# Kernel optimization log

Measured on AMD Instinct MI355X. Metric: run time of the kernel, lower is better.

Reference implementation:

```python
import jax, jax.numpy as jnp
import numpy as np

SEQ_LEN = 512
MAX_SPAN = 15
BATCH = 8
HIDDEN = 1024
WIDTH_DIM = 64
NUM_LABELS = 3


def _enumerate_spans(seq_len, max_span):
    starts, ends = [], []
    for s in range(seq_len):
        for e in range(s, min(s + max_span, seq_len)):
            starts.append(s)
            ends.append(e)
    return np.asarray(starts, np.int32), np.asarray(ends, np.int32)


def setup_inputs() -> dict:
    key = jax.random.key(0)
    k = jax.random.split(key, 6)
    starts, ends = _enumerate_spans(SEQ_LEN, MAX_SPAN)  # N = 7575
    d_in = HIDDEN * 2 + WIDTH_DIM  # 2112
    return {
        "sequence_output": jax.random.normal(k[0], (BATCH, SEQ_LEN, HIDDEN), jnp.float32),
        "width_emb": jax.random.normal(k[1], (MAX_SPAN, WIDTH_DIM), jnp.float32) * 0.02,
        "W1": jax.random.normal(k[2], (d_in, HIDDEN), jnp.float32) * (1.0 / np.sqrt(d_in)),
        "b1": jnp.zeros((HIDDEN,), jnp.float32),
        "W2": jax.random.normal(k[3], (HIDDEN, NUM_LABELS), jnp.float32) * (1.0 / np.sqrt(HIDDEN)),
        "b2": jnp.zeros((NUM_LABELS,), jnp.float32),
        "span_starts": jnp.asarray(starts),
        "span_ends": jnp.asarray(ends),
    }


def reference(sequence_output, width_emb, W1, b1, W2, b2, span_starts, span_ends):
    # Gather start/end token representations for every candidate span.
    B = sequence_output.shape[0]
    N = span_starts.shape[0]
    start_repr = sequence_output[:, span_starts]            # [B, N, H]
    end_repr = sequence_output[:, span_ends]                # [B, N, H]
    width_repr = width_emb[span_ends - span_starts]         # [N, 64]
    width_repr = jnp.broadcast_to(width_repr[None], (B, N, width_repr.shape[-1]))
    span_reprs = jnp.concatenate([start_repr, end_repr, width_repr], axis=-1)  # [B, N, 2H+64]
    # Span classifier MLP (dropout is identity in eval mode).
    h = jax.nn.relu(jnp.einsum("bnd,dh->bnh", span_reprs, W1) + b1)
    logits = jnp.einsum("bnh,hl->bnl", h, W2) + b2          # [B, N, num_labels]
    return logits
```

## Files before the change

### kernel.cpp

```cpp
#include <hip/hip_runtime.h>
#include <stdint.h>

#define SEQ 512
#define BATCH 8
#define HID 1024

typedef __attribute__((ext_vector_type(8))) __bf16 bf16x8;
typedef __attribute__((ext_vector_type(4))) float f32x4;

__device__ __forceinline__ unsigned short f2bf(float f) {
    unsigned int u = __float_as_uint(f);
    unsigned int r = 0x7fffu + ((u >> 16) & 1u);
    return (unsigned short)((u + r) >> 16);
}

__device__ __forceinline__ void unpack8(uint4 v, float* f) {
    f[0] = __uint_as_float(v.x << 16);
    f[1] = __uint_as_float(v.x & 0xffff0000u);
    f[2] = __uint_as_float(v.y << 16);
    f[3] = __uint_as_float(v.y & 0xffff0000u);
    f[4] = __uint_as_float(v.z << 16);
    f[5] = __uint_as_float(v.z & 0xffff0000u);
    f[6] = __uint_as_float(v.w << 16);
    f[7] = __uint_as_float(v.w & 0xffff0000u);
}

__global__ __launch_bounds__(256) void k_prep(const float* __restrict__ seq,
                                              const float* __restrict__ wemb,
                                              const float* __restrict__ W1,
                                              const float* __restrict__ b1,
                                              ushort* __restrict__ seqb,
                                              ushort* __restrict__ Bt,
                                              ushort* __restrict__ Rbf) {
    __shared__ float tile[32][33];
    const int bid = blockIdx.x;
    const int tid = threadIdx.x;
    if (bid < 4096) {
        int i = bid * 256 + tid;
        float4 v = ((const float4*)seq)[i];
        ushort4 o;
        o.x = f2bf(v.x); o.y = f2bf(v.y); o.z = f2bf(v.z); o.w = f2bf(v.w);
        ((ushort4*)seqb)[i] = o;
    } else if (bid < 6144) {
        int idx = bid - 4096;
        int nb = (idx & 63) * 32, kb = (idx >> 6) * 32;
        int tx = tid & 31, ty = tid >> 5;
        int n = nb + tx;
        int rb = (n < 1024) ? 0 : 1024;
        int nc = n - rb;
#pragma unroll
        for (int i = 0; i < 4; ++i) {
            int k = kb + ty + i * 8;
            tile[ty + i * 8][tx] = W1[(size_t)(rb + k) * 1024 + nc];
        }
        __syncthreads();
#pragma unroll
        for (int i = 0; i < 4; ++i) {
            int n2 = nb + ty + i * 8;
            Bt[(size_t)n2 * 1024 + kb + tx] = f2bf(tile[tx][ty + i * 8]);
        }
    } else {
        int idx = (bid - 6144) * 256 + tid;
        int w = idx >> 10, j = idx & 1023;
        float acc = b1[j];
#pragma unroll
        for (int c = 0; c < 64; ++c)
            acc = fmaf(wemb[w * 64 + c], W1[(size_t)(2048 + c) * 1024 + j], acc);
        Rbf[idx] = f2bf(acc);
    }
}

__global__ __launch_bounds__(256) void k_gemm(const ushort* __restrict__ A,
                                              const ushort* __restrict__ Bt,
                                              ushort* __restrict__ P,
                                              ushort* __restrict__ Q) {
    __shared__ ushort Al[2 * 128 * 32];
    __shared__ ushort Bl[2 * 128 * 32];
    const int tid = threadIdx.x;
    const int wid = tid >> 6;
    const int lane = tid & 63;
    const int bid = blockIdx.x;
    const int swz = ((bid & 7) << 6) | (bid >> 3);
    const int n0 = (swz & 15) * 128;
    const int m0 = (swz >> 4) * 128;
    const int wm = (wid >> 1) * 64;
    const int wn = (wid & 1) * 64;
    const int srow = lane >> 2;
    const int scol = (lane & 3) * 8;
    const int fr = lane & 15;
    const int fk = (lane >> 4) * 8;

    f32x4 acc[4][4] = {};

    for (int k0 = 0; k0 < 1024; k0 += 64) {
#pragma unroll
        for (int r = 0; r < 4; ++r) {
            int c = wid + 4 * r;
            int half = c >> 3;
            int rows = (c & 7) * 16;
            const ushort* sa = A  + (size_t)(m0 + rows + srow) * 1024 + k0 + half * 32 + scol;
            const ushort* sb = Bt + (size_t)(n0 + rows + srow) * 1024 + k0 + half * 32 + scol;
            int loff = half * 4096 + rows * 32;
            __builtin_amdgcn_global_load_lds((const __attribute__((address_space(1))) void*)sa,
                                             (__attribute__((address_space(3))) void*)(Al + loff),
                                             16, 0, 0);
            __builtin_amdgcn_global_load_lds((const __attribute__((address_space(1))) void*)sb,
                                             (__attribute__((address_space(3))) void*)(Bl + loff),
                                             16, 0, 0);
        }
        __syncthreads();
#pragma unroll
        for (int kk = 0; kk < 2; ++kk) {
            bf16x8 af[4], bg[4];
#pragma unroll
            for (int i = 0; i < 4; ++i) {
                af[i] = *(const bf16x8*)(Al + kk * 4096 + (wm + i * 16 + fr) * 32 + fk);
                bg[i] = *(const bf16x8*)(Bl + kk * 4096 + (wn + i * 16 + fr) * 32 + fk);
            }
#pragma unroll
            for (int i = 0; i < 4; ++i)
#pragma unroll
                for (int j = 0; j < 4; ++j)
                    acc[i][j] = __builtin_amdgcn_mfma_f32_16x16x32_bf16(af[i], bg[j], acc[i][j], 0, 0, 0);
        }
        __syncthreads();
    }

    ushort* Cb = (n0 < 1024) ? P : Q;
    const int nc0 = n0 & 1023;
    const int cr = (lane >> 4) * 4;
    const int cc = lane & 15;
#pragma unroll
    for (int i = 0; i < 4; ++i)
#pragma unroll
        for (int j = 0; j < 4; ++j) {
            ushort* Cp = Cb + (size_t)(m0 + wm + i * 16 + cr) * 1024 + (nc0 + wn + j * 16 + cc);
#pragma unroll
            for (int r = 0; r < 4; ++r)
                Cp[(size_t)r * 1024] = f2bf(acc[i][j][r]);
        }
}

__global__ __launch_bounds__(1024) void k_span2(const ushort* __restrict__ Pmat,
                                                const ushort* __restrict__ Qmat,
                                                const ushort* __restrict__ Rbf,
                                                const float* __restrict__ W2,
                                                const float* __restrict__ b2,
                                                float* __restrict__ out, int nspans) {
    __shared__ ushort Qs[30 * 1024];
    __shared__ ushort Rs[15 * 1024];
    const int tid = threadIdx.x;
    const int wid = tid >> 6, lane = tid & 63;
    const int b = blockIdx.x >> 5;
    const int s0 = (blockIdx.x & 31) << 4;

#pragma unroll
    for (int i = 0; i < 4; ++i) {
        int c = wid + (i << 4);
        if (c < 60) {
            int g = (c << 9) + lane * 8;
            int row = s0 + (g >> 10);
            if (row > SEQ - 1) row = SEQ - 1;
            const ushort* src = Qmat + (((size_t)(b << 9) + row) << 10) + (g & 1023);
            __builtin_amdgcn_global_load_lds((const __attribute__((address_space(1))) void*)src,
                                             (__attribute__((address_space(3))) void*)(Qs + (c << 9)),
                                             16, 0, 0);
        }
    }
#pragma unroll
    for (int i = 0; i < 2; ++i) {
        int c = wid + (i << 4);
        if (c < 30) {
            int g = (c << 9) + lane * 8;
            __builtin_amdgcn_global_load_lds((const __attribute__((address_space(1))) void*)(Rbf + g),
                                             (__attribute__((address_space(3))) void*)(Rs + (c << 9)),
                                             16, 0, 0);
        }
    }

    float w2r[3][2][8];
#pragma unroll
    for (int it = 0; it < 2; ++it)
#pragma unroll
        for (int u = 0; u < 8; ++u) {
            int j = lane * 8 + it * 512 + u;
            w2r[0][it][u] = W2[j * 3 + 0];
            w2r[1][it][u] = W2[j * 3 + 1];
            w2r[2][it][u] = W2[j * 3 + 2];
        }
    const float bb0 = b2[0], bb1 = b2[1], bb2 = b2[2];

    const int s = s0 + wid;
    float pf[16];
    {
        const uint4* pr = (const uint4*)(Pmat + (((size_t)(b << 9) + s) << 10) + lane * 8);
        unpack8(pr[0], pf);
        unpack8(pr[64], pf + 8);
    }

    __syncthreads();

    const int rrem = SEQ - s;
    const int nsp = (rrem < 15) ? rrem : 15;
    const int off = (rrem >= 15) ? 15 * s : (7575 - (rrem * (rrem + 1)) / 2);
    float* op = out + ((size_t)b * nspans + off) * 3;

    for (int w = 0; w < nsp; ++w) {
        const int erow = wid + w;
        float a0 = 0.f, a1 = 0.f, a2 = 0.f;
#pragma unroll
        for (int it = 0; it < 2; ++it) {
            uint4 qv = *(const uint4*)((const char*)Qs + erow * 2048 + it * 1024 + lane * 16);
            uint4 rv = *(const uint4*)((const char*)Rs + w * 2048 + it * 1024 + lane * 16);
            float qf[8], rf[8];
            unpack8(qv, qf);
            unpack8(rv, rf);
#pragma unroll
            for (int u = 0; u < 8; ++u) {
                float h = pf[it * 8 + u] + qf[u] + rf[u];
                h = fmaxf(h, 0.f);
                a0 = fmaf(h, w2r[0][it][u], a0);
                a1 = fmaf(h, w2r[1][it][u], a1);
                a2 = fmaf(h, w2r[2][it][u], a2);
            }
        }
#pragma unroll
        for (int o = 32; o; o >>= 1) {
            a0 += __shfl_xor(a0, o);
            a1 += __shfl_xor(a1, o);
            a2 += __shfl_xor(a2, o);
        }
        if (lane == 0) {
            op[w * 3 + 0] = a0 + bb0;
            op[w * 3 + 1] = a1 + bb1;
            op[w * 3 + 2] = a2 + bb2;
        }
    }
}

extern "C" void kernel_launch(void* const* d_in, const int* in_sizes, int n_in,
                              void* d_out, int out_size, void* d_ws, size_t ws_size,
                              hipStream_t stream) {
    const float* seq    = (const float*)d_in[0];
    const float* wemb   = (const float*)d_in[1];
    const float* W1     = (const float*)d_in[2];
    const float* b1     = (const float*)d_in[3];
    const float* W2     = (const float*)d_in[4];
    const float* b2     = (const float*)d_in[5];
    float* out = (float*)d_out;
    int nspans = in_sizes[6];

    char* ws = (char*)d_ws;
    ushort* seqb = (ushort*)ws;
    ushort* Bt   = (ushort*)(ws + (8u << 20));
    ushort* Pmat = (ushort*)(ws + (12u << 20));
    ushort* Qmat = (ushort*)(ws + (20u << 20));
    ushort* Rbf  = (ushort*)(ws + (28u << 20));

    hipLaunchKernelGGL(k_prep, dim3(6204), dim3(256), 0, stream,
                       seq, wemb, W1, b1, seqb, Bt, Rbf);
    hipLaunchKernelGGL(k_gemm, dim3(512), dim3(256), 0, stream, seqb, Bt, Pmat, Qmat);
    hipLaunchKernelGGL(k_span2, dim3(BATCH * (SEQ / 16)), dim3(1024), 0, stream,
                       Pmat, Qmat, Rbf, W2, b2, out, nspans);
}
```

Before: 62.69 us.

## Double-buffer GEMM LDS tiles and use 8 warps per block

```diff
diff --git a/kernel.cpp b/kernel.cpp
--- a/kernel.cpp
+++ b/kernel.cpp
@@ -70,12 +70,12 @@
     }
 }
 
-__global__ __launch_bounds__(256) void k_gemm(const ushort* __restrict__ A,
+__global__ __launch_bounds__(512) void k_gemm(const ushort* __restrict__ A,
                                               const ushort* __restrict__ Bt,
                                               ushort* __restrict__ P,
                                               ushort* __restrict__ Q) {
-    __shared__ ushort Al[2 * 128 * 32];
-    __shared__ ushort Bl[2 * 128 * 32];
+    __shared__ ushort Al[2][8192];
+    __shared__ ushort Bl[2][8192];
     const int tid = threadIdx.x;
     const int wid = tid >> 6;
     const int lane = tid & 63;
@@ -83,48 +83,61 @@
     const int swz = ((bid & 7) << 6) | (bid >> 3);
     const int n0 = (swz & 15) * 128;
     const int m0 = (swz >> 4) * 128;
-    const int wm = (wid >> 1) * 64;
-    const int wn = (wid & 1) * 64;
+    const int wm = (wid >> 2) * 64;
+    const int wn = (wid & 3) * 32;
     const int srow = lane >> 2;
     const int scol = (lane & 3) * 8;
     const int fr = lane & 15;
     const int fk = (lane >> 4) * 8;
 
-    f32x4 acc[4][4] = {};
-
-    for (int k0 = 0; k0 < 1024; k0 += 64) {
-#pragma unroll
-        for (int r = 0; r < 4; ++r) {
-            int c = wid + 4 * r;
-            int half = c >> 3;
-            int rows = (c & 7) * 16;
-            const ushort* sa = A  + (size_t)(m0 + rows + srow) * 1024 + k0 + half * 32 + scol;
-            const ushort* sb = Bt + (size_t)(n0 + rows + srow) * 1024 + k0 + half * 32 + scol;
-            int loff = half * 4096 + rows * 32;
-            __builtin_amdgcn_global_load_lds((const __attribute__((address_space(1))) void*)sa,
-                                             (__attribute__((address_space(3))) void*)(Al + loff),
-                                             16, 0, 0);
-            __builtin_amdgcn_global_load_lds((const __attribute__((address_space(1))) void*)sb,
-                                             (__attribute__((address_space(3))) void*)(Bl + loff),
-                                             16, 0, 0);
+    f32x4 acc[4][2] = {};
+
+    const ushort* Abase = A  + (size_t)(m0 + srow) * 1024 + scol;
+    const ushort* Bbase = Bt + (size_t)(n0 + srow) * 1024 + scol;
+
+#define STAGE(buf, k0)                                                                     \
+    {                                                                                      \
+        _Pragma("unroll")                                                                  \
+        for (int r = 0; r < 2; ++r) {                                                      \
+            int c = wid + 8 * r;                                                           \
+            int half = c >> 3;                                                             \
+            int rows = (c & 7) * 16;                                                       \
+            const ushort* sa = Abase + (size_t)rows * 1024 + (k0) + half * 32;             \
+            const ushort* sb = Bbase + (size_t)rows * 1024 + (k0) + half * 32;             \
+            int loff = half * 4096 + rows * 32;                                            \
+            __builtin_amdgcn_global_load_lds((const __attribute__((address_space(1))) void*)sa, \
+                                             (__attribute__((address_space(3))) void*)(&Al[buf][loff]), \
+                                             16, 0, 0);                                    \
+            __builtin_amdgcn_global_load_lds((const __attribute__((address_space(1))) void*)sb, \
+                                             (__attribute__((address_space(3))) void*)(&Bl[buf][loff]), \
+                                             16, 0, 0);                                    \
+        }                                                                                  \
+    }
+
+    STAGE(0, 0);
+    __syncthreads();
+
+    for (int t = 0; t < 16; ++t) {
+        const int cur = t & 1;
+        if (t < 15) STAGE(cur ^ 1, (t + 1) * 64);
+#pragma unroll
+        for (int kk = 0; kk < 2; ++kk) {
+            bf16x8 af[4], bg[2];
+#pragma unroll
+            for (int i = 0; i < 4; ++i)
+                af[i] = *(const bf16x8*)(&Al[cur][kk * 4096 + (wm + i * 16 + fr) * 32 + fk]);
+#pragma unroll
+            for (int j = 0; j < 2; ++j)
+                bg[j] = *(const bf16x8*)(&Bl[cur][kk * 4096 + (wn + j * 16 + fr) * 32 + fk]);
+#pragma unroll
+            for (int i = 0; i < 4; ++i)
+#pragma unroll
+                for (int j = 0; j < 2; ++j)
+                    acc[i][j] = __builtin_amdgcn_mfma_f32_16x16x32_bf16(af[i], bg[j], acc[i][j], 0, 0, 0);
         }
         __syncthreads();
-#pragma unroll
-        for (int kk = 0; kk < 2; ++kk) {
-            bf16x8 af[4], bg[4];
-#pragma unroll
-            for (int i = 0; i < 4; ++i) {
-                af[i] = *(const bf16x8*)(Al + kk * 4096 + (wm + i * 16 + fr) * 32 + fk);
-                bg[i] = *(const bf16x8*)(Bl + kk * 4096 + (wn + i * 16 + fr) * 32 + fk);
-            }
-#pragma unroll
-            for (int i = 0; i < 4; ++i)
-#pragma unroll
-                for (int j = 0; j < 4; ++j)
-                    acc[i][j] = __builtin_amdgcn_mfma_f32_16x16x32_bf16(af[i], bg[j], acc[i][j], 0, 0, 0);
-        }
-        __syncthreads();
-    }
+    }
+#undef STAGE
 
     ushort* Cb = (n0 < 1024) ? P : Q;
     const int nc0 = n0 & 1023;
@@ -133,7 +146,7 @@
 #pragma unroll
     for (int i = 0; i < 4; ++i)
 #pragma unroll
-        for (int j = 0; j < 4; ++j) {
+        for (int j = 0; j < 2; ++j) {
             ushort* Cp = Cb + (size_t)(m0 + wm + i * 16 + cr) * 1024 + (nc0 + wn + j * 16 + cc);
 #pragma unroll
             for (int r = 0; r < 4; ++r)
@@ -259,7 +272,7 @@
 
     hipLaunchKernelGGL(k_prep, dim3(6204), dim3(256), 0, stream,
                        seq, wemb, W1, b1, seqb, Bt, Rbf);
-    hipLaunchKernelGGL(k_gemm, dim3(512), dim3(256), 0, stream, seqb, Bt, Pmat, Qmat);
+    hipLaunchKernelGGL(k_gemm, dim3(512), dim3(512), 0, stream, seqb, Bt, Pmat, Qmat);
     hipLaunchKernelGGL(k_span2, dim3(BATCH * (SEQ / 16)), dim3(1024), 0, stream,
                        Pmat, Qmat, Rbf, W2, b2, out, nspans);
 }
```

Result: faster. 59.15 us (-5.7%).
